# Kernel optimization log

Hardware: AMD Instinct MI355X
Metric: run time of the kernel (lower is better)

The kernel has to match this reference:

```python
import jax, jax.numpy as jnp
import numpy as np

HEAD_NUM = 16
D_MODEL = 1024
D_K = D_MODEL // HEAD_NUM


def setup_inputs() -> dict:
    key = jax.random.key(0)
    ks = jax.random.split(key, 11)
    B, S = 2, 2048
    scale = 1.0 / np.sqrt(D_MODEL)
    inp = {
        'query': jax.random.normal(ks[0], (B, S, D_MODEL), jnp.float32),
        'key': jax.random.normal(ks[1], (B, S, D_MODEL), jnp.float32),
        'value': jax.random.normal(ks[2], (B, S, D_MODEL), jnp.float32),
        'W1': jax.random.normal(ks[3], (D_MODEL, D_MODEL), jnp.float32) * scale,
        'b1': jax.random.normal(ks[4], (D_MODEL,), jnp.float32) * 0.02,
        'W2': jax.random.normal(ks[5], (D_MODEL, D_MODEL), jnp.float32) * scale,
        'b2': jax.random.normal(ks[6], (D_MODEL,), jnp.float32) * 0.02,
        'W3': jax.random.normal(ks[7], (D_MODEL, D_MODEL), jnp.float32) * scale,
        'b3': jax.random.normal(ks[8], (D_MODEL,), jnp.float32) * 0.02,
        'W4': jax.random.normal(ks[9], (D_MODEL, D_MODEL), jnp.float32) * scale,
        'b4': jax.random.normal(ks[10], (D_MODEL,), jnp.float32) * 0.02,
    }
    return inp


def reference(query, key, value, W1, b1, W2, b2, W3, b3, W4, b4):
    B, S, _ = query.shape
    # linear projections (torch Linear: x @ W^T + b)
    q = query @ W1.T + b1
    k = key @ W2.T + b2
    v = value @ W3.T + b3
    # [B, H, S, d_k]
    q = q.reshape(B, S, HEAD_NUM, D_K).transpose(0, 2, 1, 3)
    k = k.reshape(B, S, HEAD_NUM, D_K).transpose(0, 2, 1, 3)
    v = v.reshape(B, S, HEAD_NUM, D_K).transpose(0, 2, 1, 3)
    # scaled dot-product attention
    scores = jnp.einsum('bhqd,bhkd->bhqk', q, k) / np.sqrt(D_K).astype(jnp.float32)
    attn = jax.nn.softmax(scores, axis=-1)
    out = jnp.einsum('bhqk,bhkd->bhqd', attn, v)
    # merge heads -> [B, S, d_model]
    out = out.transpose(0, 2, 1, 3).reshape(B, S, D_MODEL)
    result = out @ W4.T + b4
    return result
```

## Files before the change

kernel.cpp:

```cpp
#include <hip/hip_runtime.h>
#include <hip/hip_bf16.h>
#include <stdint.h>

typedef unsigned short u16;
typedef unsigned int   u32;
typedef __attribute__((ext_vector_type(4))) float f32x4;
typedef __attribute__((ext_vector_type(8))) short bf16x8;

__device__ __forceinline__ u16 f2bf(float x){
  u32 u = __float_as_uint(x);
  return (u16)((u + 0x7fffu + ((u >> 16) & 1u)) >> 16);
}

__device__ __forceinline__ u32 pkbf(float a, float b){
  __hip_bfloat162 t = __float22bfloat162_rn(make_float2(a, b));
  u32 r; __builtin_memcpy(&r, &t, 4); return r;
}

__device__ __forceinline__ float fexp2(float x){
  float r; asm("v_exp_f32 %0, %1" : "=v"(r) : "v"(x)); return r;
}

__device__ __forceinline__ void pl16swap(u32 &d, u32 &s){
  asm("v_permlane16_swap_b32 %0, %1" : "+v"(d), "+v"(s));
}

__device__ __forceinline__ bf16x8 mk8(u32 a, u32 b, u32 c, u32 d){
  union { u32 w[4]; bf16x8 v; } t; t.w[0]=a; t.w[1]=b; t.w[2]=c; t.w[3]=d; return t.v;
}

__device__ __forceinline__ void async_cp16(const void* g, void* l){
  __builtin_amdgcn_global_load_lds((const __attribute__((address_space(1))) void*)g,
                                   (__attribute__((address_space(3))) void*)l, 16, 0, 0);
}

__device__ __forceinline__ void conv_body(const float* __restrict__ x,
                                          u16* __restrict__ hi, int i){
  float4 v = *(const float4*)(x + i);
  ushort4 hv; hv.x = f2bf(v.x); hv.y = f2bf(v.y); hv.z = f2bf(v.z); hv.w = f2bf(v.w);
  *(ushort4*)(hi + i) = hv;
}

__global__ __launch_bounds__(256) void conv_all(
    const float* __restrict__ w1, const float* __restrict__ w2,
    const float* __restrict__ w3, const float* __restrict__ w4,
    u16* w1h, u16* w2h, u16* w3h, u16* w4h)
{
  const int o = blockIdx.x;
  const int z = o >> 10;
  const int blk = o & 1023;
  const float* x = (z == 0) ? w1 : (z == 1) ? w2 : (z == 2) ? w3 : w4;
  u16* y = (z == 0) ? w1h : (z == 1) ? w2h : (z == 2) ? w3h : w4h;
  conv_body(x, y, (blk * 256 + threadIdx.x) * 4);
}

__global__ __launch_bounds__(256, 3) void proj_kernel(
    const float* __restrict__ qf, const float* __restrict__ kf, const float* __restrict__ vf,
    const u16* __restrict__ w1h, const u16* __restrict__ w2h, const u16* __restrict__ w3h,
    const float* b1, const float* b2, const float* b3,
    u16* Qb, u16* Kb, u16* VbT)
{
  __shared__ u16 lA[8192];
  __shared__ u16 lB[2][8192];

  const int o = blockIdx.x;
  const int swz = (o & 7) * 96 + (o >> 3);
  const int x = swz & 7, y = (swz >> 3) & 31, z = swz >> 8;
  const float* Af; const u16* Bw; const float* bs; float sc;
  if (z == 0){ Af = qf; Bw = w1h; bs = b1; sc = 0.18033688011112042f; }
  else if (z == 1){ Af = kf; Bw = w2h; bs = b2; sc = 1.0f; }
  else { Af = vf; Bw = w3h; bs = b3; sc = 1.0f; }

  const int tid  = threadIdx.x;
  const int lane = tid & 63, wid = tid >> 6;
  const int li = lane & 15, g = lane >> 4;
  const int wr = wid >> 1, wc = wid & 1;
  const int m0 = y * 128, n0 = x * 128;

  const int r0 = tid >> 3, c0 = tid & 7;
  const size_t gsB = (size_t)r0 * 1024 + (size_t)((c0 ^ (r0 & 7)) * 8);
  const u16* pB = Bw + (size_t)n0 * 1024;

  const int ar0 = wid * 32 + (lane >> 3);
  const int ac  = lane & 7;
  const int awb = ((ac ^ (lane >> 3)) << 4);
  const float* pA = Af + (size_t)m0 * 1024;

  float4 ap[4][2];
  auto loadA = [&](int k0){
    #pragma unroll
    for (int p = 0; p < 4; p++){
      const float* s = pA + (size_t)(ar0 + 8 * p) * 1024 + k0 + ac * 8;
      ap[p][0] = *(const float4*)s;
      ap[p][1] = *(const float4*)(s + 4);
    }
  };

  f32x4 acc[4][4];
  #pragma unroll
  for (int i = 0; i < 4; i++)
    #pragma unroll
    for (int j = 0; j < 4; j++) acc[i][j] = (f32x4){0.f, 0.f, 0.f, 0.f};

  loadA(0);
  #pragma unroll
  for (int s = 0; s < 4; s++)
    async_cp16(pB + gsB + (size_t)s * 32 * 1024, (char*)lB + wid * 1024 + s * 4096);

  int cur = 0;
  for (int t = 0; t < 16; t++){
    const int k0 = t * 64;
    __builtin_amdgcn_s_barrier();
    asm volatile("s_waitcnt vmcnt(0)" ::: "memory");
    __builtin_amdgcn_sched_barrier(0);

    #pragma unroll
    for (int p = 0; p < 4; p++){
      uint4 wv;
      wv.x = pkbf(ap[p][0].x, ap[p][0].y);
      wv.y = pkbf(ap[p][0].z, ap[p][0].w);
      wv.z = pkbf(ap[p][1].x, ap[p][1].y);
      wv.w = pkbf(ap[p][1].z, ap[p][1].w);
      *(uint4*)((char*)lA + (ar0 + 8 * p) * 128 + awb) = wv;
    }
    if (t < 15){
      loadA(k0 + 64);
      #pragma unroll
      for (int s = 0; s < 4; s++)
        async_cp16(pB + gsB + (k0 + 64) + (size_t)s * 32 * 1024,
                   (char*)lB + (cur ^ 1) * 16384 + wid * 1024 + s * 4096);
    }
    asm volatile("s_waitcnt lgkmcnt(0)" ::: "memory");
    __builtin_amdgcn_sched_barrier(0);
    __builtin_amdgcn_s_barrier();

    const char* Bb = (const char*)lB + cur * 16384;
    #pragma unroll
    for (int kk = 0; kk < 2; kk++){
      bf16x8 af[4], bf4[4];
      #pragma unroll
      for (int f = 0; f < 4; f++){
        int ar = wr * 64 + f * 16 + li;
        int ja = (kk * 4 + g) ^ (ar & 7);
        af[f] = *(const bf16x8*)((const char*)lA + ar * 128 + (ja << 4));
        int br = wc * 64 + f * 16 + li;
        int jb = (kk * 4 + g) ^ (br & 7);
        bf4[f] = *(const bf16x8*)(Bb + br * 128 + (jb << 4));
      }
      __builtin_amdgcn_s_setprio(1);
      #pragma unroll
      for (int fm = 0; fm < 4; fm++)
        #pragma unroll
        for (int fn = 0; fn < 4; fn++)
          acc[fm][fn] = __builtin_amdgcn_mfma_f32_16x16x32_bf16(af[fm], bf4[fn], acc[fm][fn], 0, 0, 0);
      __builtin_amdgcn_s_setprio(0);
    }
    cur ^= 1;
  }

  float bv[4];
  #pragma unroll
  for (int fn = 0; fn < 4; fn++) bv[fn] = bs[n0 + wc * 64 + fn * 16 + li];

  if (z != 2){
    u16* out = (z == 0) ? Qb : Kb;
    #pragma unroll
    for (int fm = 0; fm < 4; fm++){
      const int mb = m0 + wr * 64 + fm * 16 + g * 4;
      #pragma unroll
      for (int fn = 0; fn < 4; fn++){
        const int n = n0 + wc * 64 + fn * 16 + li;
        #pragma unroll
        for (int r = 0; r < 4; r++)
          out[(size_t)(mb + r) * 1024 + n] = f2bf((acc[fm][fn][r] + bv[fn]) * sc);
      }
    }
  } else {
    const int bb = m0 >> 11;
    const int sq0 = (m0 & 2047) + wr * 64 + g * 4;
    #pragma unroll
    for (int fm = 0; fm < 4; fm++){
      #pragma unroll
      for (int fn = 0; fn < 4; fn++){
        const int n = n0 + wc * 64 + fn * 16 + li;
        const int hh = n >> 6, dd = n & 63;
        ushort4 hv;
        #pragma unroll
        for (int r = 0; r < 4; r++)
          ((u16*)&hv)[r] = f2bf(acc[fm][fn][r] + bv[fn]);
        size_t idx = ((size_t)(bb * 16 + hh) * 64 + dd) * 2048 + sq0 + fm * 16;
        *(ushort4*)(VbT + idx) = hv;
      }
    }
  }
}

__global__ __launch_bounds__(256, 2) void fin_kernel(
    const u16* __restrict__ A, const u16* __restrict__ B,
    const float* __restrict__ bias, float* __restrict__ out)
{
  __shared__ u16 lA[8192], lB[4096];
  const int tid  = threadIdx.x;
  const int lane = tid & 63, wid = tid >> 6;
  const int li = lane & 15, g = lane >> 4;
  const int wr = wid >> 1, wc = wid & 1;

  const int o = blockIdx.x;
  const int swz = (o & 7) * 64 + (o >> 3);
  const int x = swz & 15, y = swz >> 4;
  const int m0 = y * 128, n0 = x * 64;

  const u16* pA = A + (size_t)m0 * 1024;
  const u16* pB = B + (size_t)n0 * 1024;

  const int r0 = tid >> 3, c0 = tid & 7;
  const size_t gsrc = (size_t)r0 * 1024 + (size_t)((c0 ^ (r0 & 7)) * 8);
  char* dA = (char*)lA + wid * 1024;
  char* dB = (char*)lB + wid * 1024;

  f32x4 acc[4][2];
  #pragma unroll
  for (int i = 0; i < 4; i++)
    #pragma unroll
    for (int j = 0; j < 2; j++) acc[i][j] = (f32x4){0.f, 0.f, 0.f, 0.f};

  for (int k0 = 0; k0 < 1024; k0 += 64){
    __syncthreads();
    #pragma unroll
    for (int s = 0; s < 4; s++)
      async_cp16(pA + gsrc + k0 + (size_t)s * 32 * 1024, dA + s * 4096);
    #pragma unroll
    for (int s = 0; s < 2; s++)
      async_cp16(pB + gsrc + k0 + (size_t)s * 32 * 1024, dB + s * 4096);
    __syncthreads();

    #pragma unroll
    for (int kk = 0; kk < 2; kk++){
      bf16x8 af[4], bf2[2];
      #pragma unroll
      for (int f = 0; f < 4; f++){
        int ar = wr * 64 + f * 16 + li;
        int ja = (kk * 4 + g) ^ (ar & 7);
        af[f] = *(const bf16x8*)((const char*)lA + ar * 128 + (ja << 4));
      }
      #pragma unroll
      for (int f = 0; f < 2; f++){
        int br = wc * 32 + f * 16 + li;
        int jb = (kk * 4 + g) ^ (br & 7);
        bf2[f] = *(const bf16x8*)((const char*)lB + br * 128 + (jb << 4));
      }
      __builtin_amdgcn_s_setprio(1);
      #pragma unroll
      for (int fm = 0; fm < 4; fm++)
        #pragma unroll
        for (int fn = 0; fn < 2; fn++)
          acc[fm][fn] = __builtin_amdgcn_mfma_f32_16x16x32_bf16(af[fm], bf2[fn], acc[fm][fn], 0, 0, 0);
      __builtin_amdgcn_s_setprio(0);
    }
  }

  float bv[2];
  #pragma unroll
  for (int fn = 0; fn < 2; fn++) bv[fn] = bias[n0 + wc * 32 + fn * 16 + li];

  #pragma unroll
  for (int fm = 0; fm < 4; fm++){
    const int mb = m0 + wr * 64 + fm * 16 + g * 4;
    #pragma unroll
    for (int fn = 0; fn < 2; fn++){
      const int n = n0 + wc * 32 + fn * 16 + li;
      #pragma unroll
      for (int r = 0; r < 4; r++)
        out[(size_t)(mb + r) * 1024 + n] = acc[fm][fn][r] + bv[fn];
    }
  }
}

__global__ __launch_bounds__(256) void attn_kernel(
    const u16* __restrict__ Qb, const u16* __restrict__ Kb, const u16* __restrict__ VbT,
    u16* __restrict__ AOh)
{
  __shared__ char SL[3][16384];

  const int tid = threadIdx.x;
  const int lane = tid & 63, wid = tid >> 6;
  const int li = lane & 15, g = lane >> 4;

  const int o = blockIdx.x;
  const int swz = (o & 7) * 64 + (o >> 3);
  const int qt = swz & 15, h = (swz >> 4) & 15, b = swz >> 8;

  const int r0 = tid >> 3, ch = tid & 7;
  const int csw = (ch ^ (r0 & 7)) * 8;
  const u16* gK = Kb  + (size_t)(b * 2048 + r0) * 1024 + h * 64 + csw;
  const u16* gV = VbT + ((size_t)(b * 16 + h) * 64 + r0) * 2048 + csw;
  const int ldsW = wid * 1024;

  const int kb0 = li * 128 + ((g ^ (li & 7)) << 4);
  const int cm = ((((g & 1) << 1) | ((g >> 1) & 1)) ^ 2);
  const int vp0 = ((cm ^ (li & 7)) << 4);
  const int vp1 = (((4 + cm) ^ (li & 7)) << 4);

  const u16* qp = Qb + (size_t)(b * 2048 + qt * 128 + wid * 32 + li) * 1024 + h * 64 + g * 8;
  bf16x8 qf[2][2];
  qf[0][0] = *(const bf16x8*)(qp);
  qf[0][1] = *(const bf16x8*)(qp + 32);
  qf[1][0] = *(const bf16x8*)(qp + 16 * 1024);
  qf[1][1] = *(const bf16x8*)(qp + 16 * 1024 + 32);

  f32x4 O[2][4];
  #pragma unroll
  for (int st = 0; st < 2; st++)
    #pragma unroll
    for (int df = 0; df < 4; df++) O[st][df] = (f32x4){0.f, 0.f, 0.f, 0.f};
  f32x4 Lacc[2];
  Lacc[0] = (f32x4){0.f, 0.f, 0.f, 0.f};
  Lacc[1] = (f32x4){0.f, 0.f, 0.f, 0.f};
  const f32x4 NEGC = (f32x4){-32.f, -32.f, -32.f, -32.f};
  const u32 one2 = 0x3f803f80u;
  const bf16x8 ones = mk8(one2, one2, one2, one2);

  auto stage = [&](int t, char* buf){
    #pragma unroll
    for (int c = 0; c < 2; c++){
      async_cp16(gK + (size_t)(t * 64 + c * 32) * 1024, buf + c * 4096 + ldsW);
      async_cp16(gV + (size_t)c * 32 * 2048 + t * 64,   buf + 8192 + c * 4096 + ldsW);
    }
  };

  auto qkt = [&](const char* buf, f32x4 sc[2][4]){
    __builtin_amdgcn_s_setprio(1);
    #pragma unroll
    for (int fn = 0; fn < 4; fn++){
      bf16x8 kf0 = *(const bf16x8*)(buf + fn * 2048 + kb0);
      bf16x8 kf1 = *(const bf16x8*)(buf + fn * 2048 + (kb0 ^ 64));
      #pragma unroll
      for (int st = 0; st < 2; st++){
        f32x4 z = __builtin_amdgcn_mfma_f32_16x16x32_bf16(kf0, qf[st][0], NEGC, 0, 0, 0);
        sc[st][fn] = __builtin_amdgcn_mfma_f32_16x16x32_bf16(kf1, qf[st][1], z, 0, 0, 0);
      }
    }
    __builtin_amdgcn_s_setprio(0);
  };

  auto sfpv = [&](const f32x4 sc[2][4], const char* vbuf){
    bf16x8 pa[2][2];
    #pragma unroll
    for (int st = 0; st < 2; st++){
      float p[4][4];
      #pragma unroll
      for (int fn = 0; fn < 4; fn++)
        #pragma unroll
        for (int r = 0; r < 4; r++)
          p[fn][r] = fexp2(sc[st][fn][r]);
      #pragma unroll
      for (int ks = 0; ks < 2; ks++){
        u32 a0 = pkbf(p[2 * ks][0],     p[2 * ks][1]);
        u32 a1 = pkbf(p[2 * ks][2],     p[2 * ks][3]);
        u32 b0 = pkbf(p[2 * ks + 1][0], p[2 * ks + 1][1]);
        u32 b1 = pkbf(p[2 * ks + 1][2], p[2 * ks + 1][3]);
        pl16swap(b0, a0);
        pl16swap(b1, a1);
        pa[st][ks] = mk8(b0, b1, a0, a1);
      }
    }
    __builtin_amdgcn_s_setprio(1);
    #pragma unroll
    for (int ks = 0; ks < 2; ks++){
      Lacc[0] = __builtin_amdgcn_mfma_f32_16x16x32_bf16(ones, pa[0][ks], Lacc[0], 0, 0, 0);
      Lacc[1] = __builtin_amdgcn_mfma_f32_16x16x32_bf16(ones, pa[1][ks], Lacc[1], 0, 0, 0);
      #pragma unroll
      for (int df = 0; df < 4; df++){
        bf16x8 vf = *(const bf16x8*)(vbuf + (df * 16 + li) * 128 + (ks ? vp1 : vp0));
        O[0][df] = __builtin_amdgcn_mfma_f32_16x16x32_bf16(vf, pa[0][ks], O[0][df], 0, 0, 0);
        O[1][df] = __builtin_amdgcn_mfma_f32_16x16x32_bf16(vf, pa[1][ks], O[1][df], 0, 0, 0);
      }
    }
    __builtin_amdgcn_s_setprio(0);
  };

  char* B0 = SL[0]; char* B1 = SL[1]; char* B2 = SL[2];
  stage(0, B0);
  stage(1, B1);
  asm volatile("s_waitcnt vmcnt(4)" ::: "memory");
  __builtin_amdgcn_sched_barrier(0);
  __builtin_amdgcn_s_barrier();
  __builtin_amdgcn_sched_barrier(0);

  f32x4 sc[2][4], scN[2][4];
  qkt(B0, sc);

  for (int t = 0; t < 32; t++){
    asm volatile("s_waitcnt vmcnt(0)" ::: "memory");
    __builtin_amdgcn_sched_barrier(0);
    __builtin_amdgcn_s_barrier();
    __builtin_amdgcn_sched_barrier(0);

    if (t < 30) stage(t + 2, B2);
    if (t < 31) qkt(B1, scN);
    sfpv(sc, B0 + 8192);

    char* tmp = B0; B0 = B1; B1 = B2; B2 = tmp;
    #pragma unroll
    for (int s2 = 0; s2 < 2; s2++)
      #pragma unroll
      for (int fn = 0; fn < 4; fn++) sc[s2][fn] = scN[s2][fn];
  }

  const int rowb = b * 2048 + qt * 128 + wid * 32;
  #pragma unroll
  for (int st = 0; st < 2; st++){
    const float inv = 1.0f / Lacc[st][0];
    #pragma unroll
    for (int df = 0; df < 4; df++){
      ushort4 hv;
      #pragma unroll
      for (int r = 0; r < 4; r++)
        ((u16*)&hv)[r] = f2bf(O[st][df][r] * inv);
      size_t idx = (size_t)(rowb + st * 16 + li) * 1024 + h * 64 + df * 16 + g * 4;
      *(ushort4*)(AOh + idx) = hv;
    }
  }
}

extern "C" void kernel_launch(void* const* d_in, const int* in_sizes, int n_in,
                              void* d_out, int out_size, void* d_ws, size_t ws_size,
                              hipStream_t stream)
{
  (void)in_sizes; (void)n_in; (void)out_size; (void)ws_size;
  const float* query = (const float*)d_in[0];
  const float* key_  = (const float*)d_in[1];
  const float* value = (const float*)d_in[2];
  const float* W1 = (const float*)d_in[3];
  const float* b1 = (const float*)d_in[4];
  const float* W2 = (const float*)d_in[5];
  const float* b2 = (const float*)d_in[6];
  const float* W3 = (const float*)d_in[7];
  const float* b3 = (const float*)d_in[8];
  const float* W4 = (const float*)d_in[9];
  const float* b4 = (const float*)d_in[10];

  char* w = (char*)d_ws;
  const size_t MB = (size_t)1 << 20;
  u16* w1h = (u16*)(w + 24 * MB);
  u16* w2h = (u16*)(w + 26 * MB);
  u16* w3h = (u16*)(w + 28 * MB);
  u16* w4h = (u16*)(w + 30 * MB);
  u16* Qb  = (u16*)(w + 32 * MB);
  u16* Kb  = (u16*)(w + 40 * MB);
  u16* VbT = (u16*)(w + 56 * MB);
  u16* AOh = (u16*)(w + 64 * MB);

  conv_all<<<4096, 256, 0, stream>>>(W1, W2, W3, W4, w1h, w2h, w3h, w4h);

  proj_kernel<<<768, 256, 0, stream>>>(query, key_, value, w1h, w2h, w3h,
                                       b1, b2, b3, Qb, Kb, VbT);
  attn_kernel<<<512, 256, 0, stream>>>(Qb, Kb, VbT, AOh);
  fin_kernel<<<512, 256, 0, stream>>>(AOh, w4h, b4, (float*)d_out);
}
```

Measured before the change: 111.7 us.

## Double-buffer A tile in projection GEMM to cut per-iteration barriers

```diff
diff --git a/kernel.cpp b/kernel.cpp
--- a/kernel.cpp
+++ b/kernel.cpp
@@ -54,13 +54,13 @@
   conv_body(x, y, (blk * 256 + threadIdx.x) * 4);
 }
 
-__global__ __launch_bounds__(256, 3) void proj_kernel(
+__global__ __launch_bounds__(256, 2) void proj_kernel(
     const float* __restrict__ qf, const float* __restrict__ kf, const float* __restrict__ vf,
     const u16* __restrict__ w1h, const u16* __restrict__ w2h, const u16* __restrict__ w3h,
     const float* b1, const float* b2, const float* b3,
     u16* Qb, u16* Kb, u16* VbT)
 {
-  __shared__ u16 lA[8192];
+  __shared__ u16 lA[2][8192];
   __shared__ u16 lB[2][8192];
 
   const int o = blockIdx.x;
@@ -95,25 +95,7 @@
       ap[p][1] = *(const float4*)(s + 4);
     }
   };
-
-  f32x4 acc[4][4];
-  #pragma unroll
-  for (int i = 0; i < 4; i++)
-    #pragma unroll
-    for (int j = 0; j < 4; j++) acc[i][j] = (f32x4){0.f, 0.f, 0.f, 0.f};
-
-  loadA(0);
-  #pragma unroll
-  for (int s = 0; s < 4; s++)
-    async_cp16(pB + gsB + (size_t)s * 32 * 1024, (char*)lB + wid * 1024 + s * 4096);
-
-  int cur = 0;
-  for (int t = 0; t < 16; t++){
-    const int k0 = t * 64;
-    __builtin_amdgcn_s_barrier();
-    asm volatile("s_waitcnt vmcnt(0)" ::: "memory");
-    __builtin_amdgcn_sched_barrier(0);
-
+  auto writeA = [&](int buf){
     #pragma unroll
     for (int p = 0; p < 4; p++){
       uint4 wv;
@@ -121,19 +103,41 @@
       wv.y = pkbf(ap[p][0].z, ap[p][0].w);
       wv.z = pkbf(ap[p][1].x, ap[p][1].y);
       wv.w = pkbf(ap[p][1].z, ap[p][1].w);
-      *(uint4*)((char*)lA + (ar0 + 8 * p) * 128 + awb) = wv;
-    }
+      *(uint4*)((char*)lA + buf * 16384 + (ar0 + 8 * p) * 128 + awb) = wv;
+    }
+  };
+  auto stageB = [&](int k0, int buf){
+    #pragma unroll
+    for (int s = 0; s < 4; s++)
+      async_cp16(pB + gsB + k0 + (size_t)s * 32 * 1024,
+                 (char*)lB + buf * 16384 + wid * 1024 + s * 4096);
+  };
+
+  f32x4 acc[4][4];
+  #pragma unroll
+  for (int i = 0; i < 4; i++)
+    #pragma unroll
+    for (int j = 0; j < 4; j++) acc[i][j] = (f32x4){0.f, 0.f, 0.f, 0.f};
+
+  loadA(0);
+  __builtin_amdgcn_sched_barrier(0);
+  stageB(0, 0);
+  asm volatile("s_waitcnt vmcnt(4)" ::: "memory");
+  __builtin_amdgcn_sched_barrier(0);
+  writeA(0);
+  asm volatile("s_waitcnt vmcnt(0) lgkmcnt(0)" ::: "memory");
+  __builtin_amdgcn_sched_barrier(0);
+  __builtin_amdgcn_s_barrier();
+
+  int cur = 0;
+  for (int t = 0; t < 16; t++){
     if (t < 15){
-      loadA(k0 + 64);
-      #pragma unroll
-      for (int s = 0; s < 4; s++)
-        async_cp16(pB + gsB + (k0 + 64) + (size_t)s * 32 * 1024,
-                   (char*)lB + (cur ^ 1) * 16384 + wid * 1024 + s * 4096);
-    }
-    asm volatile("s_waitcnt lgkmcnt(0)" ::: "memory");
-    __builtin_amdgcn_sched_barrier(0);
-    __builtin_amdgcn_s_barrier();
-
+      loadA((t + 1) * 64);
+      __builtin_amdgcn_sched_barrier(0);
+      stageB((t + 1) * 64, cur ^ 1);
+    }
+
+    const char* Ab = (const char*)lA + cur * 16384;
     const char* Bb = (const char*)lB + cur * 16384;
     #pragma unroll
     for (int kk = 0; kk < 2; kk++){
@@ -142,7 +146,7 @@
       for (int f = 0; f < 4; f++){
         int ar = wr * 64 + f * 16 + li;
         int ja = (kk * 4 + g) ^ (ar & 7);
-        af[f] = *(const bf16x8*)((const char*)lA + ar * 128 + (ja << 4));
+        af[f] = *(const bf16x8*)(Ab + ar * 128 + (ja << 4));
         int br = wc * 64 + f * 16 + li;
         int jb = (kk * 4 + g) ^ (br & 7);
         bf4[f] = *(const bf16x8*)(Bb + br * 128 + (jb << 4));
@@ -155,6 +159,15 @@
           acc[fm][fn] = __builtin_amdgcn_mfma_f32_16x16x32_bf16(af[fm], bf4[fn], acc[fm][fn], 0, 0, 0);
       __builtin_amdgcn_s_setprio(0);
     }
+
+    if (t < 15){
+      asm volatile("s_waitcnt vmcnt(4)" ::: "memory");
+      __builtin_amdgcn_sched_barrier(0);
+      writeA(cur ^ 1);
+    }
+    asm volatile("s_waitcnt vmcnt(0) lgkmcnt(0)" ::: "memory");
+    __builtin_amdgcn_sched_barrier(0);
+    __builtin_amdgcn_s_barrier();
     cur ^= 1;
   }
 
```

After: 129.5 us. +16.0%, slower.
